# Kernel optimization log

Hardware: AMD Instinct MI355X
Metric: run time of the kernel (lower is better)

The kernel has to match this reference:

```python
import jax, jax.numpy as jnp
import numpy as np

N_NODES = 20000
N_EDGES = 640000
N_TRIP = 1000000
C = 128          # channels
E = 64           # expansion_features
CUTOFF = 5.0
LOG2 = float(np.log(2.0))


def ssp(x):
    # ShiftedSoftplus
    return jax.nn.softplus(x) - LOG2


def setup_inputs() -> dict:
    key = jax.random.key(0)
    ks = jax.random.split(key, 12)
    features = jax.random.normal(ks[0], (N_NODES, C), dtype=jnp.float32)
    neighbour_distances = jax.random.uniform(ks[1], (N_EDGES,), dtype=jnp.float32) * (1.2 * CUTOFF)
    neighbour_list = jax.random.randint(ks[2], (2, N_EDGES), 0, N_NODES, dtype=jnp.int32)
    triplet_idxs = jax.random.randint(ks[3], (N_TRIP, 3), 0, N_NODES, dtype=jnp.int32)
    angles = jax.random.uniform(ks[4], (N_TRIP,), dtype=jnp.float32) * np.pi
    r_ij = jax.random.uniform(ks[5], (N_TRIP,), dtype=jnp.float32) * CUTOFF
    r_ik = jax.random.uniform(ks[6], (N_TRIP,), dtype=jnp.float32) * CUTOFF
    # learned parameters (Linear layers without bias; stored [in, out])
    W_pre = jax.random.normal(ks[7], (C, C), dtype=jnp.float32) / np.sqrt(C)
    W2b1 = jax.random.normal(ks[8], (E, E), dtype=jnp.float32) / np.sqrt(E)
    W2b2 = jax.random.normal(ks[9], (E, C), dtype=jnp.float32) / np.sqrt(E)
    W3b1 = jax.random.normal(ks[10], (3, C // 2), dtype=jnp.float32) / np.sqrt(3.0)
    W3b2 = jax.random.normal(ks[11], (C // 2, C), dtype=jnp.float32) / np.sqrt(C // 2)
    W_post = jax.random.normal(jax.random.fold_in(key, 99), (C, C), dtype=jnp.float32) / np.sqrt(C)
    return {
        "features": features,
        "neighbour_distances": neighbour_distances,
        "neighbour_list": neighbour_list,
        "triplet_idxs": triplet_idxs,
        "angles": angles,
        "r_ij": r_ij,
        "r_ik": r_ik,
        "W_pre": W_pre,
        "W2b1": W2b1,
        "W2b2": W2b2,
        "W3b1": W3b1,
        "W3b2": W3b2,
        "W_post": W_post,
    }


def reference(features, neighbour_distances, neighbour_list, triplet_idxs,
              angles, r_ij, r_ik, W_pre, W2b1, W2b2, W3b1, W3b2, W_post):
    # 1) pre-linear
    h = features @ W_pre                                   # [N, C]

    # 2) radial basis (Gaussian smearing) with smooth cosine cutoff envelope
    centers = jnp.linspace(0.0, CUTOFF, E, dtype=jnp.float32)  # [E]
    width = CUTOFF / E
    gamma = 1.0 / (2.0 * width * width)
    d = neighbour_distances[:, None]                       # [n_edges, 1]
    rb = jnp.exp(-gamma * (d - centers) ** 2)              # [n_edges, E]
    cutoff_mask = (neighbour_distances < CUTOFF).astype(jnp.float32)
    cutoff_values = 0.5 * (1.0 + jnp.cos(np.pi * neighbour_distances / CUTOFF))
    rb = rb * (cutoff_values * cutoff_mask)[:, None]       # fused envelope

    # 3) two-body messages: gather neighbour node features, modulate by radial MLP
    neighbor_h = h[neighbour_list[1]]                      # [n_edges, C]
    two_body = neighbor_h * (ssp(rb @ W2b1) @ W2b2)        # [n_edges, C]

    # 4) three-body messages: angular MLP on (r_ij, r_ik, cos(angle)),
    #    gather node features at triplet_idxs[:,1], scatter-add into edge slots
    tbf = jnp.stack([r_ij, r_ik, jnp.cos(angles)], axis=-1)  # [n_trip, 3]
    w3 = ssp(tbf @ W3b1) @ W3b2                              # [n_trip, C]
    msgs = h[triplet_idxs[:, 1]] * w3                        # [n_trip, C]
    edge_msgs = jnp.zeros_like(two_body).at[triplet_idxs[:, 1]].add(msgs)

    # 5) aggregate messages over neighbours (to central atom = neighbour_list[0])
    messages = two_body + edge_msgs
    agg = jax.ops.segment_sum(messages, neighbour_list[0], num_segments=N_NODES)

    # 6) post-linear
    return agg @ W_post
```

## Files before the change

kernel.cpp:

```cpp
#include <hip/hip_runtime.h>
#include <hip/hip_fp16.h>
#include <math.h>

#define TID threadIdx.x

typedef ushort u16x8 __attribute__((ext_vector_type(8)));
typedef unsigned char uchar;

static constexpr int NN = 20000;
static constexpr int NE = 640000;
static constexpr int NT = 1000000;
static constexpr int C = 128;
static constexpr int E = 64;
static constexpr int LUTN = 4104;
static constexpr int NBKT = 625;
static constexpr int NB2 = 512;
static constexpr int CHE2 = 1250;
static constexpr int CHT2 = 1954;
static constexpr int G_GEMM = (NN + 15) / 16;
static constexpr int G_LUT = (LUTN + 7) / 8 + 1;
static constexpr int G_SCAN = (2 * NBKT + 3) / 4;
static constexpr int SCAP = 2048;
static constexpr float CUT = 5.0f;
static constexpr float LN2 = 0.69314718055994530942f;

__device__ __forceinline__ float ssp(float x) {
    return fmaxf(x, 0.0f) + __logf(1.0f + __expf(-fabsf(x))) - LN2;
}

__device__ __forceinline__ ushort f2bf(float x) {
    uint u = __float_as_uint(x);
    return (ushort)((u + 0x7FFFu + ((u >> 16) & 1u)) >> 16);
}

__device__ __forceinline__ float bf2f(ushort u) {
    return __uint_as_float((uint)u << 16);
}

__device__ __forceinline__ float h2f(uint bits) {
    return __half2float(__ushort_as_half((ushort)(bits & 0xFFFFu)));
}

__global__ __launch_bounds__(256) void k_front(const float* __restrict__ features,
                                               const float* __restrict__ W_pre,
                                               ushort* __restrict__ hB,
                                               const float* __restrict__ W2b1,
                                               const float* __restrict__ W2b2,
                                               ushort* __restrict__ lutB,
                                               float2* __restrict__ spLut,
                                               const int* __restrict__ nl0,
                                               const int* __restrict__ tidx,
                                               uchar* __restrict__ cntE,
                                               uchar* __restrict__ cntT) {
    __shared__ __align__(16) char smem[53248];
    const int bid = blockIdx.x;
    if (bid < G_GEMM) {
        ushort* wB = (ushort*)smem;
        float (*aL)[132] = (float(*)[132])(smem + 32768);
        for (int i = TID; i < C * C / 4; i += 256) {
            float4 w4 = ((const float4*)W_pre)[i];
            ushort4 u = {f2bf(w4.x), f2bf(w4.y), f2bf(w4.z), f2bf(w4.w)};
            ((ushort4*)wB)[i] = u;
        }
        const int base = bid * 16;
        for (int i = TID; i < 512; i += 256) {
            int r = base + (i >> 5);
            float4 v = (r < NN) ? ((const float4*)features)[(size_t)r * 32 + (i & 31)]
                                : (float4){0.f, 0.f, 0.f, 0.f};
            *(float4*)&aL[i >> 5][(i & 31) << 2] = v;
        }
        __syncthreads();
        const int rg = TID >> 4;
        const int c8 = (TID & 15) << 3;
        float acc[8] = {0.f, 0.f, 0.f, 0.f, 0.f, 0.f, 0.f, 0.f};
        #pragma unroll 8
        for (int k = 0; k < C; ++k) {
            float a = aL[rg][k];
            u16x8 wv = *(const u16x8*)&wB[k * C + c8];
            #pragma unroll
            for (int j = 0; j < 8; ++j) acc[j] = fmaf(a, bf2f(wv[j]), acc[j]);
        }
        int r = base + rg;
        if (r < NN) {
            u16x8 u;
            #pragma unroll
            for (int j = 0; j < 8; ++j) u[j] = f2bf(acc[j]);
            *(u16x8*)&hB[(size_t)r * C + c8] = u;
        }
        return;
    }
    if (bid < G_GEMM + G_LUT) {
        const int lb = bid - G_GEMM;
        if (lb == G_LUT - 1) {
            for (int e = TID; e < 512; e += 256) {
                float t0 = (float)e * (1.0f / 32.0f);
                float t1 = (float)(e + 1) * (1.0f / 32.0f);
                float v0 = log1pf(__expf(-t0));
                float v1 = log1pf(__expf(-t1));
                spLut[e] = make_float2(v0, v1 - v0);
            }
            return;
        }
        float* w1 = (float*)smem;
        float* w2 = (float*)(smem + 16384);
        float (*rbL)[E] = (float(*)[E])(smem + 49152);
        float (*hid)[E] = (float(*)[E])(smem + 51200);
        for (int i = TID; i < E * E; i += 256) w1[i] = W2b1[i];
        for (int i = TID; i < E * C; i += 256) w2[i] = W2b2[i];
        const int jj = TID & 63;
        const int esA = TID >> 6;
        const int eg = TID >> 5;
        const int c4 = (TID & 31) << 2;
        const float gamma = 81.92f;
        const float cstep = CUT / 63.0f;
        const float delta = CUT / 4096.0f;
        const int base = lb * 8;
        __syncthreads();
        #pragma unroll
        for (int s = 0; s < 2; ++s) {
            int es = esA + 4 * s;
            float d = (float)(base + es) * delta;
            float cv = (d < CUT) ? 0.5f * (1.0f + __cosf((float)M_PI * d / CUT)) : 0.0f;
            float dd = d - (float)jj * cstep;
            rbL[es][jj] = __expf(-gamma * dd * dd) * cv;
        }
        __syncthreads();
        #pragma unroll
        for (int s = 0; s < 2; ++s) {
            int es = esA + 4 * s;
            float a = 0.f;
            #pragma unroll 16
            for (int k = 0; k < E; ++k)
                a = fmaf(rbL[es][k], w1[k * E + jj], a);
            hid[es][jj] = ssp(a);
        }
        __syncthreads();
        float4 o = {0.f, 0.f, 0.f, 0.f};
        #pragma unroll
        for (int j = 0; j < E; ++j) {
            float t = hid[eg][j];
            const float4 w4 = *(const float4*)&w2[j * C + c4];
            o.x = fmaf(t, w4.x, o.x);
            o.y = fmaf(t, w4.y, o.y);
            o.z = fmaf(t, w4.z, o.z);
            o.w = fmaf(t, w4.w, o.w);
        }
        int row = base + eg;
        if (row < LUTN) {
            ushort4 u = {f2bf(o.x), f2bf(o.y), f2bf(o.z), f2bf(o.w)};
            *(ushort4*)&lutB[(size_t)row * C + c4] = u;
        }
        return;
    }
    {
        int* h = (int*)smem;
        const int b = bid - G_GEMM - G_LUT;
        for (int i = TID; i < NBKT; i += 256) h[i] = 0;
        __syncthreads();
        const int e0 = b * CHE2, e1 = min(e0 + CHE2, NE);
        for (int i = e0 + TID; i < e1; i += 256) atomicAdd(&h[nl0[i] >> 5], 1);
        __syncthreads();
        for (int i = TID; i < NBKT; i += 256) { cntE[(size_t)i * NB2 + b] = (uchar)h[i]; h[i] = 0; }
        __syncthreads();
        const int t0 = b * CHT2, t1 = min(t0 + CHT2, NT);
        for (int i = t0 + TID; i < t1; i += 256) atomicAdd(&h[tidx[3 * i + 1] >> 5], 1);
        __syncthreads();
        for (int i = TID; i < NBKT; i += 256) cntT[(size_t)i * NB2 + b] = (uchar)h[i];
    }
}

__global__ __launch_bounds__(256) void k_mid(const uchar* __restrict__ cE,
                                             const uchar* __restrict__ cT,
                                             ushort* __restrict__ baseE,
                                             ushort* __restrict__ baseT,
                                             int* __restrict__ totEb,
                                             int* __restrict__ totTb) {
    const int lane = TID & 63;
    const int wv = TID >> 6;
    int task = blockIdx.x * 4 + wv;
    if (task >= 2 * NBKT) return;
    const bool isE = task < NBKT;
    const int k = isE ? task : task - NBKT;
    const uchar* src = isE ? cE : cT;
    ushort* dst = isE ? baseE : baseT;
    int* dT = isE ? totEb : totTb;
    int v[8], pre[8], s = 0;
    #pragma unroll
    for (int j = 0; j < 8; ++j) {
        v[j] = src[(size_t)k * NB2 + lane * 8 + j];
        pre[j] = s;
        s += v[j];
    }
    int incl = s;
    #pragma unroll
    for (int off = 1; off < 64; off <<= 1) {
        int t = __shfl_up(incl, off, 64);
        if (lane >= off) incl += t;
    }
    int excl = incl - s;
    #pragma unroll
    for (int j = 0; j < 8; ++j)
        dst[(size_t)k * NB2 + lane * 8 + j] = (ushort)(excl + pre[j]);
    if (lane == 63) dT[k] = incl;
}

__global__ __launch_bounds__(256) void k_bplace(const int* __restrict__ nl0,
                                                const int* __restrict__ nl1,
                                                const float* __restrict__ dist,
                                                const int* __restrict__ tidx,
                                                const float* __restrict__ angles,
                                                const float* __restrict__ rij,
                                                const float* __restrict__ rik,
                                                const ushort* __restrict__ baseE,
                                                const ushort* __restrict__ baseT,
                                                const int* __restrict__ totEb,
                                                const int* __restrict__ totTb,
                                                int2* __restrict__ eT,
                                                int2* __restrict__ tT) {
    __shared__ int cur[NBKT];
    __shared__ int bksEs[NBKT];
    __shared__ int bksTs[NBKT];
    const int lane = TID & 63;
    const int wv = TID >> 6;
    if (wv < 2) {
        const int* tot = (wv == 0) ? totEb : totTb;
        int* dst = (wv == 0) ? bksEs : bksTs;
        int carry = 0;
        for (int b2 = 0; b2 < NBKT; b2 += 64) {
            int idx = b2 + lane;
            int vv = (idx < NBKT) ? tot[idx] : 0;
            int incl = vv;
            #pragma unroll
            for (int off = 1; off < 64; off <<= 1) {
                int t = __shfl_up(incl, off, 64);
                if (lane >= off) incl += t;
            }
            if (idx < NBKT) dst[idx] = carry + incl - vv;
            carry += __shfl(incl, 63, 64);
        }
    }
    __syncthreads();
    const int b = blockIdx.x;
    for (int k = TID; k < NBKT; k += 256)
        cur[k] = bksEs[k] + (int)baseE[(size_t)k * NB2 + b];
    __syncthreads();
    const int e0 = b * CHE2, e1 = min(e0 + CHE2, NE);
    for (int i = e0 + TID; i < e1; i += 256) {
        int n0 = nl0[i];
        int pos = atomicAdd(&cur[n0 >> 5], 1);
        uint tq = (uint)fmaf(dist[i], 209715.2f, 0.5f);
        eT[pos] = make_int2((int)(tq | ((uint)(n0 & 31) << 26)), nl1[i]);
    }
    __syncthreads();
    for (int k = TID; k < NBKT; k += 256)
        cur[k] = bksTs[k] + (int)baseT[(size_t)k * NB2 + b];
    __syncthreads();
    const int t0 = b * CHT2, tEnd = min(t0 + CHT2, NT);
    for (int i = t0 + TID; i < tEnd; i += 256) {
        int t1 = tidx[3 * i + 1];
        int pos = atomicAdd(&cur[t1 >> 5], 1);
        uint ab = ((uint)__half_as_ushort(__float2half_rn(rik[i])) << 16)
                | (uint)__half_as_ushort(__float2half_rn(rij[i]));
        uint cc = (uint)__half_as_ushort(__float2half_rn(__cosf(angles[i])))
                | ((uint)(t1 & 31) << 16);
        tT[pos] = make_int2((int)ab, (int)cc);
    }
}

__global__ __launch_bounds__(256) void k_sortcons(const int2* __restrict__ eT,
                                                  const int2* __restrict__ tT,
                                                  const int* __restrict__ totEb,
                                                  const int* __restrict__ totTb,
                                                  const ushort* __restrict__ hB,
                                                  const ushort* __restrict__ lutB,
                                                  const float* __restrict__ W3b1,
                                                  const float2* __restrict__ spLut,
                                                  float* __restrict__ agg,
                                                  float* __restrict__ uacc) {
    __shared__ int2 sorted[SCAP];
    __shared__ int hist[32], st[32], cur[32];
    __shared__ int bksS[NBKT];
    __shared__ uint spl[512];
    const bool isE = blockIdx.x < NBKT;
    const int bkt = isE ? blockIdx.x : blockIdx.x - NBKT;
    const int2* src = isE ? eT : tT;
    const int* totB = isE ? totEb : totTb;
    const int lane = TID & 63;
    const int wv = TID >> 6;
    for (int i = TID; i < 512; i += 256) {
        float2 vs = spLut[i];
        spl[i] = ((uint)f2bf(vs.y) << 16) | (uint)f2bf(vs.x);
    }
    if (wv == 0) {
        int carry = 0;
        for (int b2 = 0; b2 < NBKT; b2 += 64) {
            int idx = b2 + lane;
            int vv = (idx < NBKT) ? totB[idx] : 0;
            int incl = vv;
            #pragma unroll
            for (int off = 1; off < 64; off <<= 1) {
                int t = __shfl_up(incl, off, 64);
                if (lane >= off) incl += t;
            }
            if (idx < NBKT) bksS[idx] = carry + incl - vv;
            carry += __shfl(incl, 63, 64);
        }
    }
    if (TID < 32) hist[TID] = 0;
    __syncthreads();
    const int s0 = bksS[bkt];
    const int cnt = min(totB[bkt], SCAP);
    for (int i = TID; i < cnt; i += 256) {
        int2 p = src[s0 + i];
        int nlo = isE ? (int)(((uint)p.x >> 26) & 31u) : (int)(((uint)p.y >> 16) & 31u);
        atomicAdd(&hist[nlo], 1);
    }
    __syncthreads();
    if (TID < 32) {
        int v = hist[TID];
        int incl = v;
        #pragma unroll
        for (int off = 1; off < 32; off <<= 1) {
            int t = __shfl_up(incl, off, 64);
            if (TID >= off) incl += t;
        }
        st[TID] = incl - v;
        cur[TID] = incl - v;
    }
    __syncthreads();
    for (int i = TID; i < cnt; i += 256) {
        int2 p = src[s0 + i];
        int nlo = isE ? (int)(((uint)p.x >> 26) & 31u) : (int)(((uint)p.y >> 16) & 31u);
        int pos = atomicAdd(&cur[nlo], 1);
        sorted[pos] = p;
    }
    __syncthreads();
    if (isE) {
        const int c2b = lane << 2;
        for (int j = wv * 8; j < wv * 8 + 8; ++j) {
            const int s = st[j];
            const int c = hist[j];
            float a0 = 0.f, a1 = 0.f;
            #pragma unroll 4
            for (int i = 0; i < c; ++i) {
                int2 p = sorted[s + i];
                uint tq = (uint)p.x & 0x03FFFFFFu;
                int idx = min((int)(tq >> 8), LUTN - 2);
                float fr = (float)(tq & 255u) * (1.0f / 256.0f);
                ushort2 A2 = *(const ushort2*)((const char*)lutB + idx * (C * 2) + c2b);
                ushort2 B2 = *(const ushort2*)((const char*)lutB + idx * (C * 2) + 256 + c2b);
                ushort2 H2 = *(const ushort2*)((const char*)hB + p.y * (C * 2) + c2b);
                float ax = bf2f(A2.x), ay = bf2f(A2.y);
                float ox = fmaf(fr, bf2f(B2.x) - ax, ax);
                float oy = fmaf(fr, bf2f(B2.y) - ay, ay);
                a0 = fmaf(ox, bf2f(H2.x), a0);
                a1 = fmaf(oy, bf2f(H2.y), a1);
            }
            const int r = (bkt << 5) + j;
            float2 o = {a0, a1};
            *(float2*)&agg[(size_t)r * C + (lane << 1)] = o;
        }
    } else {
        const float w1a = W3b1[lane];
        const float w1b = W3b1[64 + lane];
        const float w1c = W3b1[128 + lane];
        for (int j = wv * 8; j < wv * 8 + 8; ++j) {
            const int s = st[j];
            const int c = hist[j];
            float usA = 0.f, usB = 0.f;
            int i = 0;
            #pragma unroll 4
            for (; i + 1 < c; i += 2) {
                int2 pa = sorted[s + i];
                int2 pb = sorted[s + i + 1];
                float xa = fmaf(h2f((uint)pa.x), w1a,
                          fmaf(h2f((uint)pa.x >> 16), w1b, h2f((uint)pa.y) * w1c));
                float xb = fmaf(h2f((uint)pb.x), w1a,
                          fmaf(h2f((uint)pb.x >> 16), w1b, h2f((uint)pb.y) * w1c));
                float ta = fabsf(xa) * 32.0f;
                float tb = fabsf(xb) * 32.0f;
                int ia = min((int)ta, 511);
                int ib = min((int)tb, 511);
                float fa = ta - (float)ia;
                float fb = tb - (float)ib;
                uint va = spl[ia];
                uint vb = spl[ib];
                usA += fmaxf(xa, 0.f) + fmaf(fa, bf2f((ushort)(va >> 16)), bf2f((ushort)va));
                usB += fmaxf(xb, 0.f) + fmaf(fb, bf2f((ushort)(vb >> 16)), bf2f((ushort)vb));
            }
            if (i < c) {
                int2 pa = sorted[s + i];
                float xa = fmaf(h2f((uint)pa.x), w1a,
                          fmaf(h2f((uint)pa.x >> 16), w1b, h2f((uint)pa.y) * w1c));
                float ta = fabsf(xa) * 32.0f;
                int ia = min((int)ta, 511);
                float fa = ta - (float)ia;
                uint va = spl[ia];
                usA += fmaxf(xa, 0.f) + fmaf(fa, bf2f((ushort)(va >> 16)), bf2f((ushort)va));
            }
            const int r = (bkt << 5) + j;
            uacc[(size_t)r * 64 + lane] = usA + usB - LN2 * (float)c;
        }
    }
}

__global__ __launch_bounds__(256) void k_node_final(const float* __restrict__ uacc,
                                                    const float* __restrict__ W3b2,
                                                    const ushort* __restrict__ hB,
                                                    const int* __restrict__ nl0,
                                                    float* __restrict__ agg) {
    __shared__ uint w2p[64 * 64];
    __shared__ float uL[16][68];
    for (int i = TID; i < 4096; i += 256) {
        int k = i >> 6, l = i & 63;
        w2p[i] = ((uint)f2bf(W3b2[k * C + 64 + l]) << 16) | (uint)f2bf(W3b2[k * C + l]);
    }
    const int base = blockIdx.x * 16;
    {
        int i = TID;
        int row = i >> 4, col = (i & 15) << 2;
        float4 v = ((const float4*)uacc)[(size_t)(base + row) * 16 + (i & 15)];
        *(float4*)&uL[row][col] = v;
    }
    __syncthreads();
    const int lane = TID & 63;
    const int wv = TID >> 6;
    #pragma unroll
    for (int j = 0; j < 4; ++j) {
        const int row = wv * 4 + j;
        float o0 = 0.f, o1 = 0.f;
        #pragma unroll 8
        for (int k = 0; k < 64; ++k) {
            float a = uL[row][k];
            uint wp = w2p[k * 64 + lane];
            o0 = fmaf(a, __uint_as_float(wp << 16), o0);
            o1 = fmaf(a, __uint_as_float(wp & 0xFFFF0000u), o1);
        }
        const int r = base + row;
        const int n0 = nl0[r];
        float h0 = bf2f(hB[(size_t)r * C + lane]);
        float h1 = bf2f(hB[(size_t)r * C + 64 + lane]);
        unsafeAtomicAdd(&agg[(size_t)n0 * C + lane], o0 * h0);
        unsafeAtomicAdd(&agg[(size_t)n0 * C + 64 + lane], o1 * h1);
    }
}

__global__ __launch_bounds__(256) void k_gemm16f(const float* __restrict__ A,
                                                 const float* __restrict__ W,
                                                 float* __restrict__ out, int nrows) {
    __shared__ ushort wB[C * C];
    __shared__ float aL[16][132];
    for (int i = TID; i < C * C / 4; i += 256) {
        float4 w4 = ((const float4*)W)[i];
        ushort4 u = {f2bf(w4.x), f2bf(w4.y), f2bf(w4.z), f2bf(w4.w)};
        ((ushort4*)wB)[i] = u;
    }
    const int base = blockIdx.x * 16;
    for (int i = TID; i < 512; i += 256) {
        int r = base + (i >> 5);
        float4 v = (r < nrows) ? ((const float4*)A)[(size_t)r * 32 + (i & 31)]
                               : (float4){0.f, 0.f, 0.f, 0.f};
        *(float4*)&aL[i >> 5][(i & 31) << 2] = v;
    }
    __syncthreads();
    const int rg = TID >> 4;
    const int c8 = (TID & 15) << 3;
    float acc[8] = {0.f, 0.f, 0.f, 0.f, 0.f, 0.f, 0.f, 0.f};
    #pragma unroll 8
    for (int k = 0; k < C; ++k) {
        float a = aL[rg][k];
        u16x8 wv = *(const u16x8*)&wB[k * C + c8];
        #pragma unroll
        for (int j = 0; j < 8; ++j) acc[j] = fmaf(a, bf2f(wv[j]), acc[j]);
    }
    int r = base + rg;
    if (r < nrows) {
        float4 o0 = {acc[0], acc[1], acc[2], acc[3]};
        float4 o1 = {acc[4], acc[5], acc[6], acc[7]};
        *(float4*)&out[(size_t)r * C + c8] = o0;
        *(float4*)&out[(size_t)r * C + c8 + 4] = o1;
    }
}

extern "C" void kernel_launch(void* const* d_in, const int* in_sizes, int n_in,
                              void* d_out, int out_size, void* d_ws, size_t ws_size,
                              hipStream_t stream) {
    const float* features = (const float*)d_in[0];
    const float* ndist    = (const float*)d_in[1];
    const int*   nlist    = (const int*)d_in[2];
    const int*   tidx     = (const int*)d_in[3];
    const float* angles   = (const float*)d_in[4];
    const float* rij      = (const float*)d_in[5];
    const float* rik      = (const float*)d_in[6];
    const float* W_pre    = (const float*)d_in[7];
    const float* W2b1     = (const float*)d_in[8];
    const float* W2b2     = (const float*)d_in[9];
    const float* W3b1     = (const float*)d_in[10];
    const float* W3b2     = (const float*)d_in[11];
    const float* W_post   = (const float*)d_in[12];
    float* out = (float*)d_out;

    char* w = (char*)d_ws;
    float* agg    = (float*)w;   w += (size_t)NN * C * 4;
    ushort* hB    = (ushort*)w;  w += (size_t)NN * C * 2;
    ushort* lutB  = (ushort*)w;  w += (size_t)LUTN * C * 2;
    int2* eT      = (int2*)w;    w += (size_t)NE * 8;
    int2* tT      = (int2*)w;    w += (size_t)NT * 8;
    float* uacc   = (float*)w;   w += (size_t)NN * 64 * 4;
    uchar* cntE   = (uchar*)w;   w += (size_t)NBKT * NB2;
    uchar* cntT   = (uchar*)w;   w += (size_t)NBKT * NB2;
    ushort* baseE = (ushort*)w;  w += (size_t)NBKT * NB2 * 2;
    ushort* baseT = (ushort*)w;  w += (size_t)NBKT * NB2 * 2;
    int* totEb    = (int*)w;     w += (size_t)NBKT * 4;
    int* totTb    = (int*)w;     w += (size_t)NBKT * 4;
    float2* spLut = (float2*)w;  w += 512 * 8;

    const int* nl0 = nlist;
    const int* nl1 = nlist + NE;

    hipLaunchKernelGGL(k_front, dim3(G_GEMM + G_LUT + NB2), dim3(256), 0, stream,
                       features, W_pre, hB, W2b1, W2b2, lutB, spLut,
                       nl0, tidx, cntE, cntT);
    hipLaunchKernelGGL(k_mid, dim3(G_SCAN), dim3(256), 0, stream,
                       cntE, cntT, baseE, baseT, totEb, totTb);
    hipLaunchKernelGGL(k_bplace, dim3(NB2), dim3(256), 0, stream,
                       nl0, nl1, ndist, tidx, angles, rij, rik,
                       baseE, baseT, totEb, totTb, eT, tT);
    hipLaunchKernelGGL(k_sortcons, dim3(2 * NBKT), dim3(256), 0, stream,
                       eT, tT, totEb, totTb, hB, lutB, W3b1, spLut, agg, uacc);
    hipLaunchKernelGGL(k_node_final, dim3(NN / 16), dim3(256), 0, stream,
                       uacc, W3b2, hB, nl0, agg);
    hipLaunchKernelGGL(k_gemm16f, dim3((NN + 15) / 16), dim3(256), 0, stream,
                       agg, W_post, out, NN);
}
```

Before: 168.9 us.

## Compact triplet middle indices and dynamically schedule node rows across waves

```diff
diff --git a/kernel.cpp b/kernel.cpp
--- a/kernel.cpp
+++ b/kernel.cpp
@@ -51,7 +51,8 @@
                                                const int* __restrict__ nl0,
                                                const int* __restrict__ tidx,
                                                uchar* __restrict__ cntE,
-                                               uchar* __restrict__ cntT) {
+                                               uchar* __restrict__ cntT,
+                                               int* __restrict__ t1c) {
     __shared__ __align__(16) char smem[53248];
     const int bid = blockIdx.x;
     if (bid < G_GEMM) {
@@ -163,7 +164,11 @@
         for (int i = TID; i < NBKT; i += 256) { cntE[(size_t)i * NB2 + b] = (uchar)h[i]; h[i] = 0; }
         __syncthreads();
         const int t0 = b * CHT2, t1 = min(t0 + CHT2, NT);
-        for (int i = t0 + TID; i < t1; i += 256) atomicAdd(&h[tidx[3 * i + 1] >> 5], 1);
+        for (int i = t0 + TID; i < t1; i += 256) {
+            int tv = tidx[3 * i + 1];
+            t1c[i] = tv;
+            atomicAdd(&h[tv >> 5], 1);
+        }
         __syncthreads();
         for (int i = TID; i < NBKT; i += 256) cntT[(size_t)i * NB2 + b] = (uchar)h[i];
     }
@@ -207,7 +212,7 @@
 __global__ __launch_bounds__(256) void k_bplace(const int* __restrict__ nl0,
                                                 const int* __restrict__ nl1,
                                                 const float* __restrict__ dist,
-                                                const int* __restrict__ tidx,
+                                                const int* __restrict__ t1c,
                                                 const float* __restrict__ angles,
                                                 const float* __restrict__ rij,
                                                 const float* __restrict__ rik,
@@ -257,7 +262,7 @@
     __syncthreads();
     const int t0 = b * CHT2, tEnd = min(t0 + CHT2, NT);
     for (int i = t0 + TID; i < tEnd; i += 256) {
-        int t1 = tidx[3 * i + 1];
+        int t1 = t1c[i];
         int pos = atomicAdd(&cur[t1 >> 5], 1);
         uint ab = ((uint)__half_as_ushort(__float2half_rn(rik[i])) << 16)
                 | (uint)__half_as_ushort(__float2half_rn(rij[i]));
@@ -281,6 +286,7 @@
     __shared__ int hist[32], st[32], cur[32];
     __shared__ int bksS[NBKT];
     __shared__ uint spl[512];
+    __shared__ int nextN;
     const bool isE = blockIdx.x < NBKT;
     const int bkt = isE ? blockIdx.x : blockIdx.x - NBKT;
     const int2* src = isE ? eT : tT;
@@ -307,6 +313,7 @@
         }
     }
     if (TID < 32) hist[TID] = 0;
+    if (TID == 32) nextN = 0;
     __syncthreads();
     const int s0 = bksS[bkt];
     const int cnt = min(totB[bkt], SCAP);
@@ -337,7 +344,11 @@
     __syncthreads();
     if (isE) {
         const int c2b = lane << 2;
-        for (int j = wv * 8; j < wv * 8 + 8; ++j) {
+        for (;;) {
+            int j;
+            if (lane == 0) j = atomicAdd(&nextN, 1);
+            j = __shfl(j, 0, 64);
+            if (j >= 32) break;
             const int s = st[j];
             const int c = hist[j];
             float a0 = 0.f, a1 = 0.f;
@@ -364,7 +375,11 @@
         const float w1a = W3b1[lane];
         const float w1b = W3b1[64 + lane];
         const float w1c = W3b1[128 + lane];
-        for (int j = wv * 8; j < wv * 8 + 8; ++j) {
+        for (;;) {
+            int j;
+            if (lane == 0) j = atomicAdd(&nextN, 1);
+            j = __shfl(j, 0, 64);
+            if (j >= 32) break;
             const int s = st[j];
             const int c = hist[j];
             float usA = 0.f, usB = 0.f;
@@ -507,6 +522,7 @@
     int2* eT      = (int2*)w;    w += (size_t)NE * 8;
     int2* tT      = (int2*)w;    w += (size_t)NT * 8;
     float* uacc   = (float*)w;   w += (size_t)NN * 64 * 4;
+    int* t1c      = (int*)w;     w += (size_t)NT * 4;
     uchar* cntE   = (uchar*)w;   w += (size_t)NBKT * NB2;
     uchar* cntT   = (uchar*)w;   w += (size_t)NBKT * NB2;
     ushort* baseE = (ushort*)w;  w += (size_t)NBKT * NB2 * 2;
@@ -520,11 +536,11 @@
 
     hipLaunchKernelGGL(k_front, dim3(G_GEMM + G_LUT + NB2), dim3(256), 0, stream,
                        features, W_pre, hB, W2b1, W2b2, lutB, spLut,
-                       nl0, tidx, cntE, cntT);
+                       nl0, tidx, cntE, cntT, t1c);
     hipLaunchKernelGGL(k_mid, dim3(G_SCAN), dim3(256), 0, stream,
                        cntE, cntT, baseE, baseT, totEb, totTb);
     hipLaunchKernelGGL(k_bplace, dim3(NB2), dim3(256), 0, stream,
-                       nl0, nl1, ndist, tidx, angles, rij, rik,
+                       nl0, nl1, ndist, t1c, angles, rij, rik,
                        baseE, baseT, totEb, totTb, eT, tT);
     hipLaunchKernelGGL(k_sortcons, dim3(2 * NBKT), dim3(256), 0, stream,
                        eT, tT, totEb, totTb, hB, lutB, W3b1, spLut, agg, uacc);
```

Measured after the change: 168.8 us. Within noise of the previous version (-0.1%).
